# Kernel optimization log

Measured on AMD Instinct MI355X. Metric: run time of the kernel, lower is better.

Reference implementation:

```python
import jax, jax.numpy as jnp
import numpy as np

B, S, D, H = 2, 2048, 1024, 16
DK = D // H
NEG = -1.0e9


def setup_inputs() -> dict:
    key = jax.random.key(0)
    ks = jax.random.split(key, 11)
    inp = {
        "q": jax.random.normal(ks[0], (B, S, D), jnp.float32),
        "k": jax.random.normal(ks[1], (B, S, D), jnp.float32),
        "v": jax.random.normal(ks[2], (B, S, D), jnp.float32),
        "mask": jnp.tril(jnp.ones((S, S), jnp.int32))[None, None],  # causal [1,1,S,S]
    }
    scale = 0.02
    inp["w_q"] = jax.random.normal(ks[3], (D, D), jnp.float32) * scale
    inp["b_q"] = jnp.zeros((D,), jnp.float32)
    inp["w_k"] = jax.random.normal(ks[4], (D, D), jnp.float32) * scale
    inp["b_k"] = jnp.zeros((D,), jnp.float32)
    inp["w_v"] = jax.random.normal(ks[5], (D, D), jnp.float32) * scale
    inp["b_v"] = jnp.zeros((D,), jnp.float32)
    inp["w_o"] = jax.random.normal(ks[6], (D, D), jnp.float32) * scale
    inp["b_o"] = jnp.zeros((D,), jnp.float32)
    return inp


def reference(q, k, v, mask, w_q, b_q, w_k, b_k, w_v, b_v, w_o, b_o):
    # projections: [B,S,D] -> [B,H,S,DK]
    def proj(x, w, b):
        y = jnp.einsum("bsd,de->bse", x, w) + b
        return y.reshape(B, S, H, DK).transpose(0, 2, 1, 3)

    Q = proj(q, w_q, b_q)
    K = proj(k, w_k, b_k)
    V = proj(v, w_v, b_v)
    # explicit scores matrix, faithful to the original naive attention
    scores = jnp.einsum("bhsd,bhtd->bhst", Q, K) / jnp.sqrt(jnp.float32(DK))
    scores = jnp.where(mask == 0, NEG, scores)
    attn = jax.nn.softmax(scores, axis=-1)  # dropout p=0.0 -> identity
    x = jnp.einsum("bhst,bhtd->bhsd", attn, V)
    x = x.transpose(0, 2, 1, 3).reshape(B, S, D)
    return jnp.einsum("bsd,de->bse", x, w_o) + b_o
```

## Files before the change

kernel.cpp:

```cpp
#include <hip/hip_runtime.h>
#include <hip/hip_bf16.h>

typedef __bf16 bf16;
typedef __bf16 bf16x2 __attribute__((ext_vector_type(2)));
typedef __bf16 bf16x8 __attribute__((ext_vector_type(8)));
typedef float f32x4 __attribute__((ext_vector_type(4)));
typedef float f32x16 __attribute__((ext_vector_type(16)));

#define MFMA16(a, b, c) __builtin_amdgcn_mfma_f32_16x16x32_bf16(a, b, c, 0, 0, 0)
#define MFMA32(a, b, c) __builtin_amdgcn_mfma_f32_32x32x16_bf16(a, b, c, 0, 0, 0)

#define QSCALE 0.18033688f

__device__ __forceinline__ void gld16(const bf16* g, bf16* l) {
  __builtin_amdgcn_global_load_lds(
      (const __attribute__((address_space(1))) void*)g,
      (__attribute__((address_space(3))) void*)l, 16, 0, 0);
}

__global__ __launch_bounds__(256) void convert_k(const float* __restrict__ q,
                                                 const float* __restrict__ k,
                                                 const float* __restrict__ v,
                                                 bf16* __restrict__ qb,
                                                 bf16* __restrict__ kb,
                                                 bf16* __restrict__ vb) {
  const float* src = blockIdx.y == 0 ? q : blockIdx.y == 1 ? k : v;
  bf16* dst = blockIdx.y == 0 ? qb : blockIdx.y == 1 ? kb : vb;
  const size_t i = ((size_t)blockIdx.x * 256 + threadIdx.x) * 8;
  float4 a = *(const float4*)(src + i);
  float4 b = *(const float4*)(src + i + 4);
  bf16x8 o;
  o[0] = (bf16)a.x; o[1] = (bf16)a.y; o[2] = (bf16)a.z; o[3] = (bf16)a.w;
  o[4] = (bf16)b.x; o[5] = (bf16)b.y; o[6] = (bf16)b.z; o[7] = (bf16)b.w;
  *(bf16x8*)(dst + i) = o;
}

__global__ __launch_bounds__(256) void transpose_w(const float* __restrict__ w0,
                                                   const float* __restrict__ w1,
                                                   const float* __restrict__ w2,
                                                   const float* __restrict__ w3,
                                                   bf16* __restrict__ dst) {
  __shared__ bf16 T[64][68];
  const float* W = blockIdx.z == 0 ? w0 : blockIdx.z == 1 ? w1
                   : blockIdx.z == 2 ? w2 : w3;
  bf16* Y = dst + (size_t)blockIdx.z * 1024 * 1024;
  const int t = threadIdx.x, r = t >> 2, c4 = t & 3;
  const int k0 = blockIdx.y * 64, n0 = blockIdx.x * 64;

  const float4* src = (const float4*)(W + (size_t)(k0 + r) * 1024 + n0 + c4 * 16);
  float4 f0 = src[0], f1 = src[1], f2 = src[2], f3 = src[3];
  bf16* row = &T[r][c4 * 16];
  row[0] = (bf16)f0.x; row[1] = (bf16)f0.y; row[2] = (bf16)f0.z; row[3] = (bf16)f0.w;
  row[4] = (bf16)f1.x; row[5] = (bf16)f1.y; row[6] = (bf16)f1.z; row[7] = (bf16)f1.w;
  row[8] = (bf16)f2.x; row[9] = (bf16)f2.y; row[10] = (bf16)f2.z; row[11] = (bf16)f2.w;
  row[12] = (bf16)f3.x; row[13] = (bf16)f3.y; row[14] = (bf16)f3.z; row[15] = (bf16)f3.w;
  __syncthreads();

  bf16x8 o0, o1;
#pragma unroll
  for (int j = 0; j < 8; ++j) o0[j] = T[c4 * 16 + j][r];
#pragma unroll
  for (int j = 0; j < 8; ++j) o1[j] = T[c4 * 16 + 8 + j][r];
  bf16* d = Y + (size_t)(n0 + r) * 1024 + k0 + c4 * 16;
  *(bf16x8*)d = o0;
  *(bf16x8*)(d + 8) = o1;
}

template <int QKV, int MT>
__global__ __launch_bounds__(256, 3) void gemm_p(
    const bf16* __restrict__ xq, const bf16* __restrict__ xk,
    const bf16* __restrict__ xv, const bf16* __restrict__ Wt,
    const float* __restrict__ bq, const float* __restrict__ bk,
    const float* __restrict__ bv, bf16* __restrict__ Qp,
    bf16* __restrict__ Kp, bf16* __restrict__ Vtp, float* __restrict__ Yf) {
  constexpr int AROWS = MT * 32;
  __shared__ __align__(16) bf16 SH[AROWS * 64 + 128 * 64];
  bf16* Al = SH;
  bf16* Bl = SH + AROWS * 64;

  const int z = QKV ? blockIdx.z : 0;
  const bf16* X = QKV ? (z == 0 ? xq : z == 1 ? xk : xv) : xq;
  const bf16* Bt = Wt + (size_t)z * 1048576;
  const float* bias = QKV ? (z == 0 ? bq : z == 1 ? bk : bv) : bq;
  const float escale = (QKV && z == 0) ? QSCALE : 1.0f;

  const int t = threadIdx.x;
  const int wave = t >> 6, lane = t & 63, quad = lane >> 4, l16 = lane & 15;
  const int wm = (wave >> 1) * (MT * 16), wn = (wave & 1) * 64;
  const int bm = blockIdx.y * AROWS, bn = blockIdx.x * 128;

  const int lr = (lane >> 3) & 7, lc = lane & 7;
  constexpr int NAC = AROWS / 32;
  const bf16* gA[NAC];
  bf16* lA[NAC];
#pragma unroll
  for (int i = 0; i < NAC; ++i) {
    const int q = wave * NAC + i;
    gA[i] = X + (size_t)(bm + 8 * q + lr) * 1024 + 8 * (lc ^ lr);
    lA[i] = Al + q * 512;
  }
  const bf16* gB[4];
  bf16* lB[4];
#pragma unroll
  for (int i = 0; i < 4; ++i) {
    const int q = wave * 4 + i;
    gB[i] = Bt + (size_t)(bn + 8 * q + lr) * 1024 + 8 * (lc ^ lr);
    lB[i] = Bl + q * 512;
  }

  f32x4 acc[MT][4] = {};
  const int fswz = (l16 & 7) << 4;

  for (int kb = 0; kb < 1024; kb += 64) {
    __syncthreads();
#pragma unroll
    for (int i = 0; i < NAC; ++i) gld16(gA[i] + kb, lA[i]);
#pragma unroll
    for (int i = 0; i < 4; ++i) gld16(gB[i] + kb, lB[i]);
    __syncthreads();

#pragma unroll
    for (int kk = 0; kk < 2; ++kk) {
      const int cb = (kk * 64 + quad * 16) ^ fswz;
      bf16x8 af[MT], bfr[4];
#pragma unroll
      for (int mt = 0; mt < MT; ++mt)
        af[mt] = *(const bf16x8*)((const char*)Al +
                                  (wm + mt * 16 + l16) * 128 + cb);
#pragma unroll
      for (int nt = 0; nt < 4; ++nt)
        bfr[nt] = *(const bf16x8*)((const char*)Bl +
                                   (wn + nt * 16 + l16) * 128 + cb);
#pragma unroll
      for (int mt = 0; mt < MT; ++mt)
#pragma unroll
        for (int nt = 0; nt < 4; ++nt)
          acc[mt][nt] = MFMA16(af[mt], bfr[nt], acc[mt][nt]);
    }
  }

  if (QKV && z == 2) {
    bf16* Tt = SH;
    const int b = bm >> 11;
    __syncthreads();
#pragma unroll
    for (int half = 0; half < 2; ++half) {
      if ((wave & 1) == half) {
#pragma unroll
        for (int nt = 0; nt < 4; ++nt) {
          const int ln = nt * 16 + l16;
          const float bia = bias[bn + half * 64 + ln];
#pragma unroll
          for (int mt = 0; mt < 4; ++mt)
#pragma unroll
            for (int r = 0; r < 4; ++r) {
              const int m = wm + mt * 16 + quad * 4 + r;
              Tt[ln * 136 + m] = (bf16)(acc[mt][nt][r] + bia);
            }
        }
      }
      __syncthreads();
      {
        const int ln = t >> 2, seg = (t & 3) * 32;
        const int gn = bn + half * 64 + ln;
        const int h = gn >> 6, dk = gn & 63;
        const int s0 = (bm & 2047) + seg;
        bf16* dstp = Vtp + ((size_t)(b * 16 + h) * 64 + dk) * 2048 + s0;
        const bf16* srcp = Tt + ln * 136 + seg;
#pragma unroll
        for (int j = 0; j < 4; ++j)
          *(bf16x8*)(dstp + j * 8) = *(const bf16x8*)(srcp + j * 8);
      }
      __syncthreads();
    }
  } else {
#pragma unroll
    for (int mt = 0; mt < MT; ++mt)
#pragma unroll
      for (int nt = 0; nt < 4; ++nt) {
        const int gn = bn + wn + nt * 16 + l16;
        const float bia = bias[gn];
#pragma unroll
        for (int r = 0; r < 4; ++r) {
          const int gm = bm + wm + mt * 16 + quad * 4 + r;
          const float val = (acc[mt][nt][r] + bia) * escale;
          if (!QKV) {
            Yf[(size_t)gm * 1024 + gn] = val;
          } else {
            const int b = gm >> 11, s = gm & 2047;
            const int h = gn >> 6, dk = gn & 63;
            bf16* Y = (z == 0) ? Qp : Kp;
            Y[((size_t)(b * 16 + h) * 2048 + s) * 64 + dk] = (bf16)val;
          }
        }
      }
  }
}

__global__ __launch_bounds__(256, 2) void attn_k(const bf16* __restrict__ Q,
                                                 const bf16* __restrict__ K,
                                                 const bf16* __restrict__ Vt,
                                                 bf16* __restrict__ X) {
  __shared__ __align__(16) char LB[65536];
  __shared__ float Ex[2048];
  __shared__ float ExR[128];
  __shared__ float rsL[4][32];

  bf16* KB = (bf16*)LB;
  bf16* VB = (bf16*)(LB + 32768);

  const int t = threadIdx.x;
  const int wave = t >> 6, lane = t & 63;
  const int cl = lane & 31, h = lane >> 5;
  const int qsub = wave & 1, kpart = wave >> 1;

  const int n = blockIdx.x;
  const int xcd = n & 7, mm = n >> 3;
  const int bh = xcd + 8 * (mm & 3);
  const int pairx = mm >> 2;
  const int b = bh >> 4, hh = bh & 15;

  const bf16* Qb = Q + (size_t)bh * 2048 * 64;
  const bf16* Kb = K + (size_t)bh * 2048 * 64;
  const bf16* Vb = Vt + (size_t)bh * 64 * 2048;

  const int sr = t >> 2, sc4 = t & 3;
  const int swz = (sr & 7) << 4;
  const int d0 = sr * 128 + ((sc4 * 32) ^ swz);
  const int d1 = sr * 128 + ((sc4 * 32 + 16) ^ swz);
  const int fswz = (cl & 7) << 4;

  for (int ph = 0; ph < 2; ++ph) {
    const int qt = ph ? 31 - pairx : pairx;
    const int ntiles = qt + 1;
    const int S = (ntiles + 1) >> 1;
    const int q0 = qt * 64 + qsub * 32;

    bf16x8 qf[4];
#pragma unroll
    for (int ks = 0; ks < 4; ++ks)
      qf[ks] = *(const bf16x8*)(Qb + (size_t)(q0 + cl) * 64 + ks * 16 + h * 8);

    f32x16 o0 = {}, o1 = {};
    float rs = 0.f;

#pragma unroll
    for (int p = 0; p < 2; ++p) {
      const bf16* gk = Kb + (size_t)(p * 64 + sr) * 64 + sc4 * 16;
      const bf16* gv = Vb + (size_t)sr * 2048 + p * 64 + sc4 * 16;
      bf16x8 ka = *(const bf16x8*)gk, kb2 = *(const bf16x8*)(gk + 8);
      bf16x8 va = *(const bf16x8*)gv, vb2 = *(const bf16x8*)(gv + 8);
      char* Kd = (char*)(KB + p * 4096);
      char* Vd = (char*)(VB + p * 4096);
      *(bf16x8*)(Kd + d0) = ka;  *(bf16x8*)(Kd + d1) = kb2;
      *(bf16x8*)(Vd + d0) = va;  *(bf16x8*)(Vd + d1) = vb2;
    }
    __syncthreads();

    for (int ss = 0; ss < S; ++ss) {
      const int par = ss & 1;
      const bool more = (ss + 1) < S;
      bf16x8 rk[2][2], rv[2][2];
      if (more) {
#pragma unroll
        for (int p = 0; p < 2; ++p) {
          const int kt2 = 2 * (ss + 1) + p;
          const bf16* gk = Kb + (size_t)kt2 * 4096 + sr * 64 + sc4 * 16;
          const bf16* gv = Vb + (size_t)sr * 2048 + kt2 * 64 + sc4 * 16;
          rk[p][0] = *(const bf16x8*)gk;
          rk[p][1] = *(const bf16x8*)(gk + 8);
          rv[p][0] = *(const bf16x8*)gv;
          rv[p][1] = *(const bf16x8*)(gv + 8);
        }
      }

      const int kt = 2 * ss + kpart;
      if (kt < ntiles) {
        const int k0 = kt * 64;
        const char* Kc = (const char*)(KB + (par * 2 + kpart) * 4096);
        const char* Vc = (const char*)(VB + (par * 2 + kpart) * 4096);
        const bool interior = (k0 + 63) <= q0;

        f32x16 s0v = {}, s1v = {};
#pragma unroll
        for (int ks = 0; ks < 4; ++ks) {
          const int cb = ks * 32 + h * 16;
          bf16x8 f0 = *(const bf16x8*)(Kc + cl * 128 + (cb ^ fswz));
          bf16x8 f1 = *(const bf16x8*)(Kc + (cl + 32) * 128 + (cb ^ fswz));
          s0v = MFMA32(f0, qf[ks], s0v);
          s1v = MFMA32(f1, qf[ks], s1v);
        }

        unsigned pk[8][2];
        float ts = 0.f;
        auto smax = [&](const f32x16& sv, int mk) {
#pragma unroll
          for (int sl = 0; sl < 4; ++sl)
#pragma unroll
            for (int p = 0; p < 2; ++p) {
              float e0 = exp2f(sv[sl * 4 + 2 * p]);
              float e1 = exp2f(sv[sl * 4 + 2 * p + 1]);
              if (!interior) {
                const int ky = k0 + mk * 32 + 8 * sl + 4 * h + 2 * p;
                const int qg = q0 + cl;
                if (ky > qg) e0 = 0.f;
                if (ky + 1 > qg) e1 = 0.f;
              }
              ts += e0 + e1;
              union { bf16x2 v; unsigned u; } cv;
              cv.v[0] = (bf16)e0;
              cv.v[1] = (bf16)e1;
              pk[mk * 4 + sl][p] = cv.u;
            }
        };
        smax(s0v, 0);
        smax(s1v, 1);
        rs += ts;

        bf16x8 pf[4];
#pragma unroll
        for (int ks = 0; ks < 4; ++ks) {
          const unsigned oe0 = pk[2 * ks][0], oe1 = pk[2 * ks][1];
          const unsigned oo0 = pk[2 * ks + 1][0], oo1 = pk[2 * ks + 1][1];
          const unsigned pe0 = (unsigned)__shfl_xor((int)oe0, 32, 64);
          const unsigned pe1 = (unsigned)__shfl_xor((int)oe1, 32, 64);
          const unsigned po0 = (unsigned)__shfl_xor((int)oo0, 32, 64);
          const unsigned po1 = (unsigned)__shfl_xor((int)oo1, 32, 64);
          union { unsigned u[4]; bf16x8 v; } fu;
          fu.u[0] = h ? po0 : oe0;
          fu.u[1] = h ? po1 : oe1;
          fu.u[2] = h ? oo0 : pe0;
          fu.u[3] = h ? oo1 : pe1;
          pf[ks] = fu.v;
        }

#pragma unroll
        for (int ks = 0; ks < 4; ++ks) {
          const int cb = ks * 32 + h * 16;
          bf16x8 v0f = *(const bf16x8*)(Vc + cl * 128 + (cb ^ fswz));
          bf16x8 v1f = *(const bf16x8*)(Vc + (cl + 32) * 128 + (cb ^ fswz));
          o0 = MFMA32(pf[ks], v0f, o0);
          o1 = MFMA32(pf[ks], v1f, o1);
        }
      }

      if (more) {
#pragma unroll
        for (int p = 0; p < 2; ++p) {
          char* Kd = (char*)(KB + ((par ^ 1) * 2 + p) * 4096);
          char* Vd = (char*)(VB + ((par ^ 1) * 2 + p) * 4096);
          *(bf16x8*)(Kd + d0) = rk[p][0];
          *(bf16x8*)(Kd + d1) = rk[p][1];
          *(bf16x8*)(Vd + d0) = rv[p][0];
          *(bf16x8*)(Vd + d1) = rv[p][1];
        }
      }
      __syncthreads();
    }

    if (kpart == 0) {
      float* e = Ex + qsub * 1024;
#pragma unroll
      for (int i = 0; i < 16; ++i) e[i * 64 + lane] = o0[i];
      ExR[qsub * 64 + lane] = rs;
    }
    __syncthreads();
    if (kpart == 1) {
      const float* e = Ex + qsub * 1024;
#pragma unroll
      for (int i = 0; i < 16; ++i) o0[i] += e[i * 64 + lane];
      rs += ExR[qsub * 64 + lane];
    }
    __syncthreads();
    if (kpart == 0) {
      float* e = Ex + qsub * 1024;
#pragma unroll
      for (int i = 0; i < 16; ++i) e[i * 64 + lane] = o1[i];
    }
    __syncthreads();
    if (kpart == 1) {
      const float* e = Ex + qsub * 1024;
#pragma unroll
      for (int i = 0; i < 16; ++i) o1[i] += e[i * 64 + lane];

      const float rtot = rs + __shfl_xor(rs, 32, 64);
      rsL[wave][cl] = 1.0f / rtot;
      __builtin_amdgcn_s_waitcnt(0xC07F);
      bf16* Xb = X + (size_t)b * 2048 * 1024 + hh * 64;
#pragma unroll
      for (int g = 0; g < 16; ++g) {
        const int qr = (g & 3) + 8 * (g >> 2) + 4 * h;
        const float ri = rsL[wave][qr];
        const int qg = q0 + qr;
        Xb[(size_t)qg * 1024 + cl] = (bf16)(o0[g] * ri);
        Xb[(size_t)qg * 1024 + 32 + cl] = (bf16)(o1[g] * ri);
      }
    }
    __syncthreads();
  }
}

extern "C" void kernel_launch(void* const* d_in, const int* in_sizes, int n_in,
                              void* d_out, int out_size, void* d_ws,
                              size_t ws_size, hipStream_t stream) {
  const float* q = (const float*)d_in[0];
  const float* k = (const float*)d_in[1];
  const float* v = (const float*)d_in[2];
  const float* w_q = (const float*)d_in[4];
  const float* b_q = (const float*)d_in[5];
  const float* w_k = (const float*)d_in[6];
  const float* b_k = (const float*)d_in[7];
  const float* w_v = (const float*)d_in[8];
  const float* b_v = (const float*)d_in[9];
  const float* w_o = (const float*)d_in[10];
  const float* b_o = (const float*)d_in[11];

  bf16* ws = (bf16*)d_ws;
  const size_t NELEM = (size_t)4096 * 1024;
  bf16* Qp = ws;
  bf16* Kp = ws + NELEM;
  bf16* Vtp = ws + 2 * NELEM;
  bf16* Xp = ws + 3 * NELEM;
  bf16* Wt = ws + 4 * NELEM;
  bf16* Wto = Wt + 3145728;
  bf16* qb = Xp;
  bf16* kb = (bf16*)d_out;
  bf16* vb = kb + NELEM;

  convert_k<<<dim3(2048, 3), 256, 0, stream>>>(q, k, v, qb, kb, vb);
  transpose_w<<<dim3(16, 16, 4), 256, 0, stream>>>(w_q, w_k, w_v, w_o, Wt);

  gemm_p<1, 4><<<dim3(8, 32, 3), 256, 0, stream>>>(
      qb, kb, vb, Wt, b_q, b_k, b_v, Qp, Kp, Vtp, nullptr);
  attn_k<<<dim3(512), 256, 0, stream>>>(Qp, Kp, Vtp, Xp);
  gemm_p<0, 2><<<dim3(8, 64), 256, 0, stream>>>(
      Xp, nullptr, nullptr, Wto, b_o, nullptr, nullptr, nullptr, nullptr,
      nullptr, (float*)d_out);
}
```

Before: 227.8 us.

## Fuse fp32-to-bf16 input conversion into QKV projection GEMM A-tile loads

Removes the separate convert_k kernel. The QKV projection GEMM now reads fp32 activations straight into registers, converts them to bf16, and writes them into swizzled LDS. The next k-tile is prefetched into registers while the current one is computed. This saves one kernel launch and a round trip of the bf16 copies through global memory, but each GEMM block now reads fp32 A data (twice the bytes, re-read by all 8 column blocks) and uses more registers in exchange.

```diff
diff --git a/kernel.cpp b/kernel.cpp
--- a/kernel.cpp
+++ b/kernel.cpp
@@ -16,23 +16,6 @@
   __builtin_amdgcn_global_load_lds(
       (const __attribute__((address_space(1))) void*)g,
       (__attribute__((address_space(3))) void*)l, 16, 0, 0);
-}
-
-__global__ __launch_bounds__(256) void convert_k(const float* __restrict__ q,
-                                                 const float* __restrict__ k,
-                                                 const float* __restrict__ v,
-                                                 bf16* __restrict__ qb,
-                                                 bf16* __restrict__ kb,
-                                                 bf16* __restrict__ vb) {
-  const float* src = blockIdx.y == 0 ? q : blockIdx.y == 1 ? k : v;
-  bf16* dst = blockIdx.y == 0 ? qb : blockIdx.y == 1 ? kb : vb;
-  const size_t i = ((size_t)blockIdx.x * 256 + threadIdx.x) * 8;
-  float4 a = *(const float4*)(src + i);
-  float4 b = *(const float4*)(src + i + 4);
-  bf16x8 o;
-  o[0] = (bf16)a.x; o[1] = (bf16)a.y; o[2] = (bf16)a.z; o[3] = (bf16)a.w;
-  o[4] = (bf16)b.x; o[5] = (bf16)b.y; o[6] = (bf16)b.z; o[7] = (bf16)b.w;
-  *(bf16x8*)(dst + i) = o;
 }
 
 __global__ __launch_bounds__(256) void transpose_w(const float* __restrict__ w0,
@@ -68,18 +51,19 @@
 
 template <int QKV, int MT>
 __global__ __launch_bounds__(256, 3) void gemm_p(
-    const bf16* __restrict__ xq, const bf16* __restrict__ xk,
-    const bf16* __restrict__ xv, const bf16* __restrict__ Wt,
-    const float* __restrict__ bq, const float* __restrict__ bk,
-    const float* __restrict__ bv, bf16* __restrict__ Qp,
-    bf16* __restrict__ Kp, bf16* __restrict__ Vtp, float* __restrict__ Yf) {
+    const float* __restrict__ xq, const float* __restrict__ xk,
+    const float* __restrict__ xv, const bf16* __restrict__ xo,
+    const bf16* __restrict__ Wt, const float* __restrict__ bq,
+    const float* __restrict__ bk, const float* __restrict__ bv,
+    bf16* __restrict__ Qp, bf16* __restrict__ Kp, bf16* __restrict__ Vtp,
+    float* __restrict__ Yf) {
   constexpr int AROWS = MT * 32;
   __shared__ __align__(16) bf16 SH[AROWS * 64 + 128 * 64];
   bf16* Al = SH;
   bf16* Bl = SH + AROWS * 64;
 
   const int z = QKV ? blockIdx.z : 0;
-  const bf16* X = QKV ? (z == 0 ? xq : z == 1 ? xk : xv) : xq;
+  const float* Xf = QKV ? (z == 0 ? xq : z == 1 ? xk : xv) : nullptr;
   const bf16* Bt = Wt + (size_t)z * 1048576;
   const float* bias = QKV ? (z == 0 ? bq : z == 1 ? bk : bv) : bq;
   const float escale = (QKV && z == 0) ? QSCALE : 1.0f;
@@ -90,15 +74,6 @@
   const int bm = blockIdx.y * AROWS, bn = blockIdx.x * 128;
 
   const int lr = (lane >> 3) & 7, lc = lane & 7;
-  constexpr int NAC = AROWS / 32;
-  const bf16* gA[NAC];
-  bf16* lA[NAC];
-#pragma unroll
-  for (int i = 0; i < NAC; ++i) {
-    const int q = wave * NAC + i;
-    gA[i] = X + (size_t)(bm + 8 * q + lr) * 1024 + 8 * (lc ^ lr);
-    lA[i] = Al + q * 512;
-  }
   const bf16* gB[4];
   bf16* lB[4];
 #pragma unroll
@@ -108,16 +83,66 @@
     lB[i] = Bl + q * 512;
   }
 
+  const int arow = t >> 1, ahalf = t & 1;
+  const float* gAf =
+      QKV ? (Xf + (size_t)(bm + arow) * 1024 + ahalf * 32) : nullptr;
+  bf16* aw[4];
+#pragma unroll
+  for (int j = 0; j < 4; ++j)
+    aw[j] = (bf16*)((char*)Al + arow * 128 +
+                    (((ahalf * 4 + j) ^ (arow & 7)) << 4));
+  constexpr int NAC = AROWS / 32;
+  const bf16* gA[NAC];
+  bf16* lA[NAC];
+#pragma unroll
+  for (int i = 0; i < NAC; ++i) {
+    const int q = wave * NAC + i;
+    gA[i] = (QKV ? (const bf16*)nullptr
+                 : xo + (size_t)(bm + 8 * q + lr) * 1024 + 8 * (lc ^ lr));
+    lA[i] = Al + q * 512;
+  }
+
   f32x4 acc[MT][4] = {};
   const int fswz = (l16 & 7) << 4;
 
+  float4 rA[8];
+  if constexpr (QKV) {
+#pragma unroll
+    for (int j = 0; j < 4; ++j) {
+      rA[2 * j] = *(const float4*)(gAf + 8 * j);
+      rA[2 * j + 1] = *(const float4*)(gAf + 8 * j + 4);
+    }
+  }
+
   for (int kb = 0; kb < 1024; kb += 64) {
     __syncthreads();
-#pragma unroll
-    for (int i = 0; i < NAC; ++i) gld16(gA[i] + kb, lA[i]);
+    if constexpr (QKV) {
+#pragma unroll
+      for (int j = 0; j < 4; ++j) {
+        bf16x8 o;
+        o[0] = (bf16)rA[2 * j].x; o[1] = (bf16)rA[2 * j].y;
+        o[2] = (bf16)rA[2 * j].z; o[3] = (bf16)rA[2 * j].w;
+        o[4] = (bf16)rA[2 * j + 1].x; o[5] = (bf16)rA[2 * j + 1].y;
+        o[6] = (bf16)rA[2 * j + 1].z; o[7] = (bf16)rA[2 * j + 1].w;
+        *(bf16x8*)aw[j] = o;
+      }
+    } else {
+#pragma unroll
+      for (int i = 0; i < NAC; ++i) gld16(gA[i] + kb, lA[i]);
+    }
 #pragma unroll
     for (int i = 0; i < 4; ++i) gld16(gB[i] + kb, lB[i]);
     __syncthreads();
+
+    if constexpr (QKV) {
+      if (kb + 64 < 1024) {
+#pragma unroll
+        for (int j = 0; j < 4; ++j) {
+          rA[2 * j] = *(const float4*)(gAf + kb + 64 + 8 * j);
+          rA[2 * j + 1] = *(const float4*)(gAf + kb + 64 + 8 * j + 4);
+        }
+      }
+    }
 
 #pragma unroll
     for (int kk = 0; kk < 2; ++kk) {
@@ -423,17 +448,13 @@
   bf16* Xp = ws + 3 * NELEM;
   bf16* Wt = ws + 4 * NELEM;
   bf16* Wto = Wt + 3145728;
-  bf16* qb = Xp;
-  bf16* kb = (bf16*)d_out;
-  bf16* vb = kb + NELEM;
-
-  convert_k<<<dim3(2048, 3), 256, 0, stream>>>(q, k, v, qb, kb, vb);
+
   transpose_w<<<dim3(16, 16, 4), 256, 0, stream>>>(w_q, w_k, w_v, w_o, Wt);
 
   gemm_p<1, 4><<<dim3(8, 32, 3), 256, 0, stream>>>(
-      qb, kb, vb, Wt, b_q, b_k, b_v, Qp, Kp, Vtp, nullptr);
+      q, k, v, nullptr, Wt, b_q, b_k, b_v, Qp, Kp, Vtp, nullptr);
   attn_k<<<dim3(512), 256, 0, stream>>>(Qp, Kp, Vtp, Xp);
   gemm_p<0, 2><<<dim3(8, 64), 256, 0, stream>>>(
-      Xp, nullptr, nullptr, Wto, b_o, nullptr, nullptr, nullptr, nullptr,
-      nullptr, (float*)d_out);
+      nullptr, nullptr, nullptr, Xp, Wto, b_o, nullptr, nullptr, nullptr,
+      nullptr, nullptr, (float*)d_out);
 }
```

Measured after the change: 247.5 us. +8.7%, slower.

## Merge input prep kernels and skip fully masked half of diagonal tiles

Applied to the files above, without the earlier changes.

Combines the fp32-to-bf16 conversion and weight transpose into a single prep launch, with conversion blocks each handling eight chunks, which removes one kernel launch. In the attention kernel, when a key tile starts exactly at the query tile start, the upper 32 keys lie entirely above the causal diagonal for the warp's rows, so their QK and PV MFMAs and softmax work are skipped. This cuts work only on diagonal tiles and adds some branching and code size.

```diff
diff --git a/kernel.cpp b/kernel.cpp
--- a/kernel.cpp
+++ b/kernel.cpp
@@ -18,33 +18,36 @@
       (__attribute__((address_space(3))) void*)l, 16, 0, 0);
 }
 
-__global__ __launch_bounds__(256) void convert_k(const float* __restrict__ q,
-                                                 const float* __restrict__ k,
-                                                 const float* __restrict__ v,
-                                                 bf16* __restrict__ qb,
-                                                 bf16* __restrict__ kb,
-                                                 bf16* __restrict__ vb) {
-  const float* src = blockIdx.y == 0 ? q : blockIdx.y == 1 ? k : v;
-  bf16* dst = blockIdx.y == 0 ? qb : blockIdx.y == 1 ? kb : vb;
-  const size_t i = ((size_t)blockIdx.x * 256 + threadIdx.x) * 8;
-  float4 a = *(const float4*)(src + i);
-  float4 b = *(const float4*)(src + i + 4);
-  bf16x8 o;
-  o[0] = (bf16)a.x; o[1] = (bf16)a.y; o[2] = (bf16)a.z; o[3] = (bf16)a.w;
-  o[4] = (bf16)b.x; o[5] = (bf16)b.y; o[6] = (bf16)b.z; o[7] = (bf16)b.w;
-  *(bf16x8*)(dst + i) = o;
-}
-
-__global__ __launch_bounds__(256) void transpose_w(const float* __restrict__ w0,
-                                                   const float* __restrict__ w1,
-                                                   const float* __restrict__ w2,
-                                                   const float* __restrict__ w3,
-                                                   bf16* __restrict__ dst) {
+__global__ __launch_bounds__(256) void prep_k(
+    const float* __restrict__ w0, const float* __restrict__ w1,
+    const float* __restrict__ w2, const float* __restrict__ w3,
+    bf16* __restrict__ dst, const float* __restrict__ q,
+    const float* __restrict__ k, const float* __restrict__ v,
+    bf16* __restrict__ qb, bf16* __restrict__ kb, bf16* __restrict__ vb) {
+  const int t = threadIdx.x;
+  if (blockIdx.z >= 4) {
+    const int zi = blockIdx.z - 4;
+    const float* src = zi == 0 ? q : zi == 1 ? k : v;
+    bf16* d = zi == 0 ? qb : zi == 1 ? kb : vb;
+    const int fb = blockIdx.y * 16 + blockIdx.x;
+#pragma unroll
+    for (int j = 0; j < 8; ++j) {
+      const size_t i = ((size_t)j * 65536 + fb * 256 + t) * 8;
+      float4 a = *(const float4*)(src + i);
+      float4 b = *(const float4*)(src + i + 4);
+      bf16x8 o;
+      o[0] = (bf16)a.x; o[1] = (bf16)a.y; o[2] = (bf16)a.z; o[3] = (bf16)a.w;
+      o[4] = (bf16)b.x; o[5] = (bf16)b.y; o[6] = (bf16)b.z; o[7] = (bf16)b.w;
+      *(bf16x8*)(d + i) = o;
+    }
+    return;
+  }
+
   __shared__ bf16 T[64][68];
   const float* W = blockIdx.z == 0 ? w0 : blockIdx.z == 1 ? w1
                    : blockIdx.z == 2 ? w2 : w3;
   bf16* Y = dst + (size_t)blockIdx.z * 1024 * 1024;
-  const int t = threadIdx.x, r = t >> 2, c4 = t & 3;
+  const int r = t >> 2, c4 = t & 3;
   const int k0 = blockIdx.y * 64, n0 = blockIdx.x * 64;
 
   const float4* src = (const float4*)(W + (size_t)(k0 + r) * 1024 + n0 + c4 * 16);
@@ -280,20 +283,26 @@
         const char* Kc = (const char*)(KB + (par * 2 + kpart) * 4096);
         const char* Vc = (const char*)(VB + (par * 2 + kpart) * 4096);
         const bool interior = (k0 + 63) <= q0;
+        const bool skipHi = (k0 == q0);
 
         f32x16 s0v = {}, s1v = {};
 #pragma unroll
         for (int ks = 0; ks < 4; ++ks) {
           const int cb = ks * 32 + h * 16;
           bf16x8 f0 = *(const bf16x8*)(Kc + cl * 128 + (cb ^ fswz));
-          bf16x8 f1 = *(const bf16x8*)(Kc + (cl + 32) * 128 + (cb ^ fswz));
           s0v = MFMA32(f0, qf[ks], s0v);
-          s1v = MFMA32(f1, qf[ks], s1v);
-        }
-
-        unsigned pk[8][2];
+        }
+        if (!skipHi) {
+#pragma unroll
+          for (int ks = 0; ks < 4; ++ks) {
+            const int cb = ks * 32 + h * 16;
+            bf16x8 f1 = *(const bf16x8*)(Kc + (cl + 32) * 128 + (cb ^ fswz));
+            s1v = MFMA32(f1, qf[ks], s1v);
+          }
+        }
+
         float ts = 0.f;
-        auto smax = [&](const f32x16& sv, int mk) {
+        auto smax = [&](const f32x16& sv, int mk, unsigned (&out)[4][2]) {
 #pragma unroll
           for (int sl = 0; sl < 4; ++sl)
 #pragma unroll
@@ -310,18 +319,16 @@
               union { bf16x2 v; unsigned u; } cv;
               cv.v[0] = (bf16)e0;
               cv.v[1] = (bf16)e1;
-              pk[mk * 4 + sl][p] = cv.u;
+              out[sl][p] = cv.u;
             }
         };
-        smax(s0v, 0);
-        smax(s1v, 1);
-        rs += ts;
-
-        bf16x8 pf[4];
-#pragma unroll
-        for (int ks = 0; ks < 4; ++ks) {
-          const unsigned oe0 = pk[2 * ks][0], oe1 = pk[2 * ks][1];
-          const unsigned oo0 = pk[2 * ks + 1][0], oo1 = pk[2 * ks + 1][1];
+
+        unsigned pkLo[4][2];
+        smax(s0v, 0, pkLo);
+
+        auto mkpf = [&](const unsigned (&pk)[4][2], int ks2) -> bf16x8 {
+          const unsigned oe0 = pk[2 * ks2][0], oe1 = pk[2 * ks2][1];
+          const unsigned oo0 = pk[2 * ks2 + 1][0], oo1 = pk[2 * ks2 + 1][1];
           const unsigned pe0 = (unsigned)__shfl_xor((int)oe0, 32, 64);
           const unsigned pe1 = (unsigned)__shfl_xor((int)oe1, 32, 64);
           const unsigned po0 = (unsigned)__shfl_xor((int)oo0, 32, 64);
@@ -331,17 +338,37 @@
           fu.u[1] = h ? po1 : oe1;
           fu.u[2] = h ? oo0 : pe0;
           fu.u[3] = h ? oo1 : pe1;
-          pf[ks] = fu.v;
-        }
-
-#pragma unroll
-        for (int ks = 0; ks < 4; ++ks) {
+          return fu.v;
+        };
+        bf16x8 pfLo[2];
+        pfLo[0] = mkpf(pkLo, 0);
+        pfLo[1] = mkpf(pkLo, 1);
+
+#pragma unroll
+        for (int ks = 0; ks < 2; ++ks) {
           const int cb = ks * 32 + h * 16;
           bf16x8 v0f = *(const bf16x8*)(Vc + cl * 128 + (cb ^ fswz));
           bf16x8 v1f = *(const bf16x8*)(Vc + (cl + 32) * 128 + (cb ^ fswz));
-          o0 = MFMA32(pf[ks], v0f, o0);
-          o1 = MFMA32(pf[ks], v1f, o1);
-        }
+          o0 = MFMA32(pfLo[ks], v0f, o0);
+          o1 = MFMA32(pfLo[ks], v1f, o1);
+        }
+
+        if (!skipHi) {
+          unsigned pkHi[4][2];
+          smax(s1v, 1, pkHi);
+          bf16x8 pfHi[2];
+          pfHi[0] = mkpf(pkHi, 0);
+          pfHi[1] = mkpf(pkHi, 1);
+#pragma unroll
+          for (int ks = 2; ks < 4; ++ks) {
+            const int cb = ks * 32 + h * 16;
+            bf16x8 v0f = *(const bf16x8*)(Vc + cl * 128 + (cb ^ fswz));
+            bf16x8 v1f = *(const bf16x8*)(Vc + (cl + 32) * 128 + (cb ^ fswz));
+            o0 = MFMA32(pfHi[ks - 2], v0f, o0);
+            o1 = MFMA32(pfHi[ks - 2], v1f, o1);
+          }
+        }
+        rs += ts;
       }
 
       if (more) {
@@ -427,8 +454,8 @@
   bf16* kb = (bf16*)d_out;
   bf16* vb = kb + NELEM;
 
-  convert_k<<<dim3(2048, 3), 256, 0, stream>>>(q, k, v, qb, kb, vb);
-  transpose_w<<<dim3(16, 16, 4), 256, 0, stream>>>(w_q, w_k, w_v, w_o, Wt);
+  prep_k<<<dim3(16, 16, 7), 256, 0, stream>>>(w_q, w_k, w_v, w_o, Wt, q, k, v,
+                                              qb, kb, vb);
 
   gemm_p<1, 4><<<dim3(8, 32, 3), 256, 0, stream>>>(
       qb, kb, vb, Wt, b_q, b_k, b_v, Qp, Kp, Vtp, nullptr);
```

After: 228.1 us. No clear change (+0.2%).
